# Kernel tuning notes

Hardware: AMD Instinct MI355X
Metric: run time of the kernel (lower is better)

The kernel has to match this reference:

```python
import jax, jax.numpy as jnp
import numpy as np

DIM = 512
HEADS = 8
TOP_K = 16


def setup_inputs() -> dict:
    key = jax.random.key(0)
    ks = jax.random.split(key, 7)
    B, N, C = 8, 1024, DIM
    std = 0.02
    return {
        "x": jax.random.normal(ks[0], (B, N, C), dtype=jnp.float32),
        "Wq": jax.random.normal(ks[1], (C, C), dtype=jnp.float32) * std,
        "bq": jnp.zeros((C,), dtype=jnp.float32),
        "Wkv": jax.random.normal(ks[2], (C, 2 * C), dtype=jnp.float32) * std,
        "bkv": jnp.zeros((2 * C,), dtype=jnp.float32),
        "Wp": jax.random.normal(ks[3], (C, C), dtype=jnp.float32) * std,
        "bp": jnp.zeros((C,), dtype=jnp.float32),
    }


def reference(x, Wq, bq, Wkv, bkv, Wp, bp):
    B, N, C = x.shape
    H = HEADS
    D = C // H
    scale = D ** (-0.5)

    # q: [B,H,N,D], ReLU-activated
    q = (x @ Wq + bq).reshape(B, N, H, D).transpose(0, 2, 1, 3)
    q = jax.nn.relu(q)
    # kv: [B,N,2,H,D] -> k,v each [B,H,N,D]
    kv = (x @ Wkv + bkv).reshape(B, N, 2, H, D).transpose(2, 0, 3, 1, 4)
    k, v = kv[0], kv[1]

    # dense scores [B,H,N,N]
    attn = jnp.einsum('bhnd,bhmd->bhnm', q, k) * scale

    # top-k mask along last dim (scatter ones at topk indices)
    _, idx = jax.lax.top_k(attn, TOP_K)            # [B,H,N,K]
    flat_attn = attn.reshape(-1, N)
    flat_idx = idx.reshape(-1, TOP_K)
    rows = jnp.arange(flat_attn.shape[0])[:, None]
    mask = jnp.zeros_like(flat_attn).at[rows, flat_idx].set(1.0).reshape(attn.shape)

    # NOTE: faithful to the original - softmax over the full row of attn*mask
    # (masked-out entries contribute exp(0)=1, exactly as in the torch code)
    sparse_attn = jax.nn.softmax(attn * mask, axis=-1)

    out = jnp.einsum('bhnm,bhmd->bhnd', sparse_attn, v)
    out = out.transpose(0, 2, 1, 3).reshape(B, N, C)
    out = out @ Wp + bp
    return out
```

## Files before the change

kernel.cpp:

```cpp
#include <hip/hip_runtime.h>
#include <float.h>

#define BATCH 8
#define SEQ   1024
#define CDIM  512
#define HEADS 8
#define HD    64
#define TOPK  16
#define MTOT  (BATCH*SEQ)

typedef short bf16x8 __attribute__((ext_vector_type(8)));
typedef float f32x4v __attribute__((ext_vector_type(4)));
typedef unsigned int __attribute__((address_space(1))) guint;
typedef unsigned int __attribute__((address_space(3))) luint;

__device__ inline void bf16split(float f, unsigned short& h, unsigned short& l) {
    unsigned u = __float_as_uint(f);
    unsigned hr = (u + 0x7fffu + ((u >> 16) & 1u)) >> 16;
    h = (unsigned short)hr;
    float rest = f - __uint_as_float(hr << 16);
    unsigned v = __float_as_uint(rest);
    l = (unsigned short)((v + 0x7fffu + ((v >> 16) & 1u)) >> 16);
}

__global__ __launch_bounds__(256) void split_x_kernel(
    const float* __restrict__ x,
    unsigned short* __restrict__ xhi, unsigned short* __restrict__ xlo)
{
    size_t i = ((size_t)blockIdx.x * 256 + threadIdx.x) * 4;
    float4 v = *(const float4*)(x + i);
    ushort4 h, l;
    bf16split(v.x, h.x, l.x); bf16split(v.y, h.y, l.y);
    bf16split(v.z, h.z, l.z); bf16split(v.w, h.w, l.w);
    *(ushort4*)(xhi + i) = h;
    *(ushort4*)(xlo + i) = l;
}

__global__ __launch_bounds__(256) void split_wT_kernel(
    const float* __restrict__ Wq, const float* __restrict__ Wkv,
    const float* __restrict__ Wp,
    unsigned short* __restrict__ bThi, unsigned short* __restrict__ bTlo,
    unsigned short* __restrict__ wpThi, unsigned short* __restrict__ wpTlo)
{
    __shared__ float tile[64][65];
    const int ct = blockIdx.x, k0 = blockIdx.y * 64, t = threadIdx.x;
    const float* src; int ld, sc0, dr0;
    unsigned short *dhi, *dlo;
    if (ct < 8)       { src = Wq;  ld = CDIM;     sc0 = ct * 64;        dr0 = ct * 64;              dhi = bThi;  dlo = bTlo;  }
    else if (ct < 24) { src = Wkv; ld = 2 * CDIM; sc0 = (ct - 8) * 64;  dr0 = CDIM + (ct - 8) * 64; dhi = bThi;  dlo = bTlo;  }
    else              { src = Wp;  ld = CDIM;     sc0 = (ct - 24) * 64; dr0 = (ct - 24) * 64;       dhi = wpThi; dlo = wpTlo; }

    #pragma unroll
    for (int i = 0; i < 4; i++) {
        int f = t + i * 256;
        int r = f >> 4, c4 = f & 15;
        float4 v = *(const float4*)(src + (size_t)(k0 + r) * ld + sc0 + c4 * 4);
        tile[c4*4+0][r] = v.x; tile[c4*4+1][r] = v.y;
        tile[c4*4+2][r] = v.z; tile[c4*4+3][r] = v.w;
    }
    __syncthreads();
    #pragma unroll
    for (int i = 0; i < 2; i++) {
        int f = t + i * 256;
        int c = f >> 3, ko = f & 7;
        const float* tp = &tile[c][ko * 8];
        ushort4 h0, l0, h1, l1;
        bf16split(tp[0], h0.x, l0.x); bf16split(tp[1], h0.y, l0.y);
        bf16split(tp[2], h0.z, l0.z); bf16split(tp[3], h0.w, l0.w);
        bf16split(tp[4], h1.x, l1.x); bf16split(tp[5], h1.y, l1.y);
        bf16split(tp[6], h1.z, l1.z); bf16split(tp[7], h1.w, l1.w);
        size_t o = (size_t)(dr0 + c) * CDIM + k0 + ko * 8;
        *(ushort4*)(dhi + o)     = h0; *(ushort4*)(dhi + o + 4) = h1;
        *(ushort4*)(dlo + o)     = l0; *(ushort4*)(dlo + o + 4) = l1;
    }
}

__device__ __forceinline__ void mfma_gemm_core(
    const unsigned short* __restrict__ ahi, const unsigned short* __restrict__ alo,
    const unsigned short* __restrict__ bhi, const unsigned short* __restrict__ blo,
    int row0, int col0, int lane, int w, f32x4v acc[4][4])
{
    __shared__ __align__(16) unsigned short ah_s[4096], al_s[4096];
    __shared__ __align__(16) unsigned short bh_s[4096], bl_s[4096];

    const unsigned short* gsrc;
    unsigned short* lbase;
    if (w == 0)      { gsrc = ahi; lbase = ah_s; }
    else if (w == 1) { gsrc = alo; lbase = al_s; }
    else if (w == 2) { gsrc = bhi; lbase = bh_s; }
    else             { gsrc = blo; lbase = bl_s; }
    const int tile0 = (w < 2) ? row0 : col0;
    const size_t goff = (size_t)(tile0 + (lane & 15)) * CDIM + (lane >> 4) * 8;
    const int wr = w >> 1, wc = w & 1;

    #pragma unroll
    for (int i = 0; i < 4; i++)
        #pragma unroll
        for (int j = 0; j < 4; j++)
            acc[i][j] = (f32x4v){0.f, 0.f, 0.f, 0.f};

    for (int kt = 0; kt < CDIM; kt += 32) {
        #pragma unroll
        for (int c = 0; c < 8; c++)
            __builtin_amdgcn_global_load_lds(
                (const guint*)(gsrc + goff + kt + (size_t)c * 16 * CDIM),
                (luint*)(lbase + c * 512), 16, 0, 0);
        __syncthreads();

        bf16x8 afh[4], afl[4], bfh[4], bfl[4];
        #pragma unroll
        for (int i = 0; i < 4; i++) {
            afh[i] = *(const bf16x8*)&ah_s[(((wr*4 + i) * 64) + lane) * 8];
            afl[i] = *(const bf16x8*)&al_s[(((wr*4 + i) * 64) + lane) * 8];
            bfh[i] = *(const bf16x8*)&bh_s[(((wc*4 + i) * 64) + lane) * 8];
            bfl[i] = *(const bf16x8*)&bl_s[(((wc*4 + i) * 64) + lane) * 8];
        }
        #pragma unroll
        for (int i = 0; i < 4; i++)
            #pragma unroll
            for (int j = 0; j < 4; j++) {
                acc[i][j] = __builtin_amdgcn_mfma_f32_16x16x32_bf16(bfh[j], afh[i], acc[i][j], 0, 0, 0);
                acc[i][j] = __builtin_amdgcn_mfma_f32_16x16x32_bf16(bfh[j], afl[i], acc[i][j], 0, 0, 0);
                acc[i][j] = __builtin_amdgcn_mfma_f32_16x16x32_bf16(bfl[j], afh[i], acc[i][j], 0, 0, 0);
            }
        __syncthreads();
    }
}

__global__ __launch_bounds__(256) void qkv_mfma_kernel(
    const unsigned short* __restrict__ xhi, const unsigned short* __restrict__ xlo,
    const unsigned short* __restrict__ bThi, const unsigned short* __restrict__ bTlo,
    const float* __restrict__ bq, const float* __restrict__ bkv,
    unsigned short* __restrict__ qhi_g, unsigned short* __restrict__ qlo_g,
    unsigned short* __restrict__ khi_g, unsigned short* __restrict__ klo_g,
    float* __restrict__ v_ws)
{
    const int tid = threadIdx.x, lane = tid & 63, w = tid >> 6;
    const int row0 = blockIdx.x * 128, col0 = blockIdx.y * 128;

    f32x4v acc[4][4];
    mfma_gemm_core(xhi, xlo, bThi, bTlo, row0, col0, lane, w, acc);

    const int wr = w >> 1, wc = w & 1;
    const bool isq = (col0 < CDIM);
    #pragma unroll
    for (int i = 0; i < 4; i++) {
        int rG = row0 + (wr*4 + i) * 16 + (lane & 15);
        int bb = rG >> 10, nn = rG & (SEQ - 1);
        #pragma unroll
        for (int j = 0; j < 4; j++) {
            int cG = col0 + (wc*4 + j) * 16 + (lane >> 4) * 4;
            float4 bias4 = isq ? *(const float4*)(bq + cG)
                               : *(const float4*)(bkv + cG - CDIM);
            float4 val;
            val.x = acc[i][j][0] + bias4.x;
            val.y = acc[i][j][1] + bias4.y;
            val.z = acc[i][j][2] + bias4.z;
            val.w = acc[i][j][3] + bias4.w;
            if (isq) {
                val.x = fmaxf(val.x, 0.f); val.y = fmaxf(val.y, 0.f);
                val.z = fmaxf(val.z, 0.f); val.w = fmaxf(val.w, 0.f);
                int hq = cG >> 6, d = cG & 63;
                size_t base = (((size_t)bb * HEADS + hq) * SEQ + nn) * HD + d;
                ushort4 hv, lv;
                bf16split(val.x, hv.x, lv.x); bf16split(val.y, hv.y, lv.y);
                bf16split(val.z, hv.z, lv.z); bf16split(val.w, hv.w, lv.w);
                *(ushort4*)(qhi_g + base) = hv;
                *(ushort4*)(qlo_g + base) = lv;
            } else {
                int c2 = cG - CDIM;
                int t = c2 >> 9, hq = (c2 >> 6) & 7, d = c2 & 63;
                size_t base = (((size_t)bb * HEADS + hq) * SEQ + nn) * HD + d;
                if (t == 0) {
                    ushort4 hv, lv;
                    bf16split(val.x, hv.x, lv.x); bf16split(val.y, hv.y, lv.y);
                    bf16split(val.z, hv.z, lv.z); bf16split(val.w, hv.w, lv.w);
                    *(ushort4*)(khi_g + base) = hv;
                    *(ushort4*)(klo_g + base) = lv;
                } else {
                    *(float4*)(v_ws + base) = val;
                }
            }
        }
    }
}

__global__ __launch_bounds__(256) void vsum_kernel(
    const float* __restrict__ v_ws, float* __restrict__ vsum_ws)
{
    __shared__ float red[4][HD];
    const int bh = blockIdx.x;
    const int d  = threadIdx.x & 63;
    const int sl = threadIdx.x >> 6;
    const float* vh = v_ws + (size_t)bh * SEQ * HD;
    float s = 0.f;
    for (int m = sl * 256; m < (sl + 1) * 256; m++) s += vh[(size_t)m * HD + d];
    red[sl][d] = s;
    __syncthreads();
    if (threadIdx.x < HD)
        vsum_ws[(size_t)bh * HD + d] = red[0][d] + red[1][d] + red[2][d] + red[3][d];
}

__global__ __launch_bounds__(256) void score_kernel(
    const unsigned short* __restrict__ qhi_g, const unsigned short* __restrict__ qlo_g,
    const unsigned short* __restrict__ khi_g, const unsigned short* __restrict__ klo_g,
    float* __restrict__ s_g, int bh0)
{
    __shared__ __align__(16) short qhi_s[4096], qlo_s[4096];
    __shared__ __align__(16) short khi_s[2][4096], klo_s[2][4096];

    const int bhl = blockIdx.y;
    const int bh  = bh0 + bhl;
    const int n0  = blockIdx.x * 64;
    const int tid = threadIdx.x;
    const int lane = tid & 63, w = tid >> 6;
    const int r_st = tid >> 2, c4 = tid & 3;
    const size_t hb = (size_t)bh * SEQ * HD;

    const int s0 = c4 * 2, s1 = s0 + 1;
    const int cx0 = ((r_st >> 4)*2 + (s0 >> 2))*64 + (s0 & 3)*16 + (r_st & 15);
    const int cx1 = ((r_st >> 4)*2 + (s1 >> 2))*64 + (s1 & 3)*16 + (r_st & 15);

    {
        const unsigned short* qp  = qhi_g + hb + (size_t)(n0 + r_st)*HD + c4*16;
        const unsigned short* qp2 = qlo_g + hb + (size_t)(n0 + r_st)*HD + c4*16;
        uint4 h0 = *(const uint4*)qp,  h1 = *(const uint4*)(qp + 8);
        uint4 l0 = *(const uint4*)qp2, l1 = *(const uint4*)(qp2 + 8);
        *(uint4*)&qhi_s[cx0*8] = h0; *(uint4*)&qhi_s[cx1*8] = h1;
        *(uint4*)&qlo_s[cx0*8] = l0; *(uint4*)&qlo_s[cx1*8] = l1;
    }
    __syncthreads();
    bf16x8 qh[2], ql[2];
    #pragma unroll
    for (int h = 0; h < 2; h++) {
        qh[h] = *(bf16x8*)&qhi_s[((w*2 + h)*64 + lane)*8];
        ql[h] = *(bf16x8*)&qlo_s[((w*2 + h)*64 + lane)*8];
    }

    {
        const unsigned short* kp  = khi_g + hb + (size_t)r_st*HD + c4*16;
        const unsigned short* kp2 = klo_g + hb + (size_t)r_st*HD + c4*16;
        uint4 kh0 = *(const uint4*)kp,  kh1 = *(const uint4*)(kp + 8);
        uint4 kl0 = *(const uint4*)kp2, kl1 = *(const uint4*)(kp2 + 8);
        *(uint4*)&khi_s[0][cx0*8] = kh0; *(uint4*)&khi_s[0][cx1*8] = kh1;
        *(uint4*)&klo_s[0][cx0*8] = kl0; *(uint4*)&klo_s[0][cx1*8] = kl1;
    }
    __syncthreads();

    float* srow_base = s_g + ((size_t)bhl << 20);

    for (int mt = 0; mt < SEQ / 64; mt++) {
        const int cur = mt & 1, nxt = cur ^ 1;
        uint4 kh0, kh1, kl0, kl1;
        if (mt + 1 < SEQ / 64) {
            const unsigned short* kp  = khi_g + hb + (size_t)((mt+1)*64 + r_st)*HD + c4*16;
            const unsigned short* kp2 = klo_g + hb + (size_t)((mt+1)*64 + r_st)*HD + c4*16;
            kh0 = *(const uint4*)kp;  kh1 = *(const uint4*)(kp + 8);
            kl0 = *(const uint4*)kp2; kl1 = *(const uint4*)(kp2 + 8);
        }

        #pragma unroll
        for (int ct = 0; ct < 4; ct++) {
            f32x4v acc = {0.f, 0.f, 0.f, 0.f};
            #pragma unroll
            for (int h = 0; h < 2; h++) {
                bf16x8 kfh = *(bf16x8*)&khi_s[cur][((ct*2 + h)*64 + lane)*8];
                bf16x8 kfl = *(bf16x8*)&klo_s[cur][((ct*2 + h)*64 + lane)*8];
                acc = __builtin_amdgcn_mfma_f32_16x16x32_bf16(qh[h], kfh, acc, 0, 0, 0);
                acc = __builtin_amdgcn_mfma_f32_16x16x32_bf16(qh[h], kfl, acc, 0, 0, 0);
                acc = __builtin_amdgcn_mfma_f32_16x16x32_bf16(ql[h], kfh, acc, 0, 0, 0);
            }
            const int col  = mt*64 + ct*16 + (lane & 15);
            const int rowb = n0 + w*16 + (lane >> 4)*4;
            float* sp = srow_base + ((size_t)rowb << 10) + col;
            #pragma unroll
            for (int rg = 0; rg < 4; rg++)
                sp[(size_t)rg << 10] = acc[rg] * 0.125f;
        }

        if (mt + 1 < SEQ / 64) {
            *(uint4*)&khi_s[nxt][cx0*8] = kh0; *(uint4*)&khi_s[nxt][cx1*8] = kh1;
            *(uint4*)&klo_s[nxt][cx0*8] = kl0; *(uint4*)&klo_s[nxt][cx1*8] = kl1;
        }
        __syncthreads();
    }
}

__device__ __forceinline__ unsigned long long packkey(float f, int gidx) {
    unsigned u = __float_as_uint(f);
    unsigned o = u ^ ((unsigned)((int)u >> 31) | 0x80000000u);
    return ((unsigned long long)o << 32) | (unsigned)(~gidx);
}

struct TopCache { unsigned long long t0, t1, t2, t3; int cnt; };

__device__ __forceinline__ void cache_insert(TopCache& c, unsigned long long k) {
    bool b0 = k > c.t0, b1 = k > c.t1, b2 = k > c.t2, b3 = k > c.t3;
    c.t3 = b3 ? (b2 ? c.t2 : k) : c.t3;
    c.t2 = b2 ? (b1 ? c.t1 : k) : c.t2;
    c.t1 = b1 ? (b0 ? c.t0 : k) : c.t1;
    c.t0 = b0 ? k : c.t0;
}

__device__ __forceinline__ void cache_build(TopCache& c, const float* v, int gbase) {
    c.t0 = c.t1 = c.t2 = c.t3 = 0ull;
    #pragma unroll
    for (int j = 0; j < 16; j++) cache_insert(c, packkey(v[j], gbase + j));
    c.cnt = 4;
}

__device__ __forceinline__ void cache_pop_own(TopCache& c, bool own) {
    c.t0 = own ? c.t1 : c.t0;
    c.t1 = own ? c.t2 : c.t1;
    c.t2 = own ? c.t3 : c.t2;
    c.t3 = own ? 0ull : c.t3;
    c.cnt -= own;
}

__device__ __forceinline__ void cache_refill(TopCache& c, const float* v,
                                             int gbase, unsigned long long kw) {
    c.t0 = c.t1 = c.t2 = c.t3 = 0ull;
    int cc = 0;
    #pragma unroll
    for (int j = 0; j < 16; j++) {
        unsigned long long k = packkey(v[j], gbase + j);
        if (k < kw) { cc++; cache_insert(c, k); }
    }
    c.cnt = cc > 4 ? 4 : cc;
}

__device__ __forceinline__ unsigned umax2(unsigned a, unsigned b) { return a > b ? a : b; }

__device__ __forceinline__ unsigned wave_max_ord(unsigned o) {
    unsigned p;
    p = (unsigned)__builtin_amdgcn_update_dpp(0, (int)o, 0xB1, 0xF, 0xF, true); o = umax2(o, p);
    p = (unsigned)__builtin_amdgcn_update_dpp(0, (int)o, 0x4E, 0xF, 0xF, true); o = umax2(o, p);
    p = (unsigned)__builtin_amdgcn_ds_swizzle((int)o, 0x101F); o = umax2(o, p);
    p = (unsigned)__builtin_amdgcn_ds_swizzle((int)o, 0x201F); o = umax2(o, p);
    p = (unsigned)__builtin_amdgcn_ds_swizzle((int)o, 0x401F); o = umax2(o, p);
    p = (unsigned)__shfl_xor((int)o, 32);                      o = umax2(o, p);
    return o;
}

__device__ __forceinline__ float ord_to_float(unsigned o) {
    return __uint_as_float(o ^ ((unsigned)((int)(~o) >> 31) | 0x80000000u));
}

__global__ __launch_bounds__(256) void topk_pv_kernel(
    const float* __restrict__ s_g, const float* __restrict__ v_ws,
    const float* __restrict__ vsum_ws,
    unsigned short* __restrict__ aohi, unsigned short* __restrict__ aolo, int bh0)
{
    const int lane = threadIdx.x & 63;
    const int wid  = (blockIdx.x * 256 + threadIdx.x) >> 6;
    const int bhl  = wid >> 9;
    const int pr   = wid & 511;
    const int nA   = pr * 2;
    const int bh   = bh0 + bhl;
    const int gbase = lane * 16;

    const float* srowA = s_g + ((size_t)bhl << 20) + ((size_t)nA << 10) + gbase;
    const float* srowB = srowA + SEQ;
    float vA[16], vB[16];
    #pragma unroll
    for (int i = 0; i < 4; i++) {
        float4 ta = *(const float4*)(srowA + i * 4);
        vA[i*4+0] = ta.x; vA[i*4+1] = ta.y; vA[i*4+2] = ta.z; vA[i*4+3] = ta.w;
        float4 tb = *(const float4*)(srowB + i * 4);
        vB[i*4+0] = tb.x; vB[i*4+1] = tb.y; vB[i*4+2] = tb.z; vB[i*4+3] = tb.w;
    }

    TopCache cA, cB;
    cache_build(cA, vA, gbase);
    cache_build(cB, vB, gbase);

    const float* vh = v_ws + ((size_t)bh << 16);
    const float vs = vsum_ws[(bh << 6) + lane];

    float mxA, eA, ZA, SA, mxB, eB, ZB, SB;

    {
        unsigned oA = (unsigned)(cA.t0 >> 32);
        unsigned oB = (unsigned)(cB.t0 >> 32);
        unsigned mA = wave_max_ord(oA);
        unsigned mB = wave_max_ord(oB);
        unsigned long long blA = __ballot(oA == mA);
        unsigned long long blB = __ballot(oB == mB);
        int sA = __ffsll(blA) - 1;
        int sB = __ffsll(blB) - 1;
        unsigned loA = (unsigned)__builtin_amdgcn_readlane((int)(unsigned)cA.t0, sA);
        unsigned loB = (unsigned)__builtin_amdgcn_readlane((int)(unsigned)cB.t0, sB);
        float valA = ord_to_float(mA), valB = ord_to_float(mB);
        int idxA = (int)((~loA) & 1023u);
        int idxB = (int)((~loB) & 1023u);

        mxA = fmaxf(valA, 0.f); eA = __expf(-mxA);
        float wEA = __expf(valA - mxA);
        ZA = (float)(SEQ - TOPK) * eA + wEA;
        SA = (wEA - eA) * vh[((size_t)idxA << 6) + lane];

        mxB = fmaxf(valB, 0.f); eB = __expf(-mxB);
        float wEB = __expf(valB - mxB);
        ZB = (float)(SEQ - TOPK) * eB + wEB;
        SB = (wEB - eB) * vh[((size_t)idxB << 6) + lane];

        cache_pop_own(cA, lane == sA);
        cache_pop_own(cB, lane == sB);
    }

    #pragma unroll 1
    for (int t = 1; t < TOPK; t++) {
        unsigned oA = (unsigned)(cA.t0 >> 32);
        unsigned oB = (unsigned)(cB.t0 >> 32);
        unsigned mA = wave_max_ord(oA);
        unsigned mB = wave_max_ord(oB);
        unsigned long long blA = __ballot(oA == mA);
        unsigned long long blB = __ballot(oB == mB);
        int sA = __ffsll(blA) - 1;
        int sB = __ffsll(blB) - 1;
        unsigned loA = (unsigned)__builtin_amdgcn_readlane((int)(unsigned)cA.t0, sA);
        unsigned loB = (unsigned)__builtin_amdgcn_readlane((int)(unsigned)cB.t0, sB);
        float valA = ord_to_float(mA), valB = ord_to_float(mB);
        int idxA = (int)((~loA) & 1023u);
        int idxB = (int)((~loB) & 1023u);

        float wEA = __expf(valA - mxA);
        ZA += wEA;
        SA = fmaf(wEA - eA, vh[((size_t)idxA << 6) + lane], SA);

        float wEB = __expf(valB - mxB);
        ZB += wEB;
        SB = fmaf(wEB - eB, vh[((size_t)idxB << 6) + lane], SB);

        cache_pop_own(cA, lane == sA);
        cache_pop_own(cB, lane == sB);

        if (cA.cnt == 0 && t < TOPK - 1) {
            unsigned long long kwA = ((unsigned long long)mA << 32) | loA;
            cache_refill(cA, vA, gbase, kwA);
        }
        if (cB.cnt == 0 && t < TOPK - 1) {
            unsigned long long kwB = ((unsigned long long)mB << 32) | loB;
            cache_refill(cB, vB, gbase, kwB);
        }
    }

    float accA = (eA * vs + SA) / ZA;
    float accB = (eB * vs + SB) / ZB;

    const int b = bh >> 3, hh = bh & 7;
    size_t oA = (((size_t)b << 10) + nA) * CDIM + (hh << 6) + lane;
    unsigned short sh, sl;
    bf16split(accA, sh, sl);
    aohi[oA] = sh; aolo[oA] = sl;
    bf16split(accB, sh, sl);
    aohi[oA + CDIM] = sh; aolo[oA + CDIM] = sl;
}

__global__ __launch_bounds__(256) void proj_mfma_kernel(
    const unsigned short* __restrict__ aohi, const unsigned short* __restrict__ aolo,
    const unsigned short* __restrict__ wpThi, const unsigned short* __restrict__ wpTlo,
    const float* __restrict__ bp, float* __restrict__ out)
{
    const int tid = threadIdx.x, lane = tid & 63, w = tid >> 6;
    const int row0 = blockIdx.x * 128, col0 = blockIdx.y * 128;

    f32x4v acc[4][4];
    mfma_gemm_core(aohi, aolo, wpThi, wpTlo, row0, col0, lane, w, acc);

    const int wr = w >> 1, wc = w & 1;
    #pragma unroll
    for (int i = 0; i < 4; i++) {
        int rG = row0 + (wr*4 + i) * 16 + (lane & 15);
        #pragma unroll
        for (int j = 0; j < 4; j++) {
            int cG = col0 + (wc*4 + j) * 16 + (lane >> 4) * 4;
            float4 b4 = *(const float4*)(bp + cG);
            float4 val;
            val.x = acc[i][j][0] + b4.x;
            val.y = acc[i][j][1] + b4.y;
            val.z = acc[i][j][2] + b4.z;
            val.w = acc[i][j][3] + b4.w;
            *(float4*)(out + (size_t)rG * CDIM + cG) = val;
        }
    }
}

extern "C" void kernel_launch(void* const* d_in, const int* in_sizes, int n_in,
                              void* d_out, int out_size, void* d_ws, size_t ws_size,
                              hipStream_t stream)
{
    const float* x   = (const float*)d_in[0];
    const float* Wq  = (const float*)d_in[1];
    const float* bq  = (const float*)d_in[2];
    const float* Wkv = (const float*)d_in[3];
    const float* bkv = (const float*)d_in[4];
    const float* Wp  = (const float*)d_in[5];
    const float* bp  = (const float*)d_in[6];
    float* out = (float*)d_out;

    const size_t HSZ = (size_t)BATCH * HEADS * SEQ * HD;
    float* ws    = (float*)d_ws;
    float* v_ws  = ws;
    float* vs_ws = ws + HSZ;
    unsigned short* qhi_g = (unsigned short*)(ws + HSZ + 4096);
    unsigned short* qlo_g = qhi_g + HSZ;
    unsigned short* khi_g = qhi_g + 2 * HSZ;
    unsigned short* klo_g = qhi_g + 3 * HSZ;
    unsigned short* xhi_g = qhi_g + 4 * HSZ;
    unsigned short* xlo_g = qhi_g + 5 * HSZ;
    unsigned short* bThi  = qhi_g + 6 * HSZ;
    unsigned short* bTlo  = bThi + (size_t)1536 * 512;
    unsigned short* wpThi = bThi + (size_t)2 * 1536 * 512;
    unsigned short* wpTlo = wpThi + (size_t)512 * 512;

    const size_t plane_us = 6 * HSZ + (size_t)2 * 1536 * 512 + (size_t)2 * 512 * 512;
    const size_t base_fl  = HSZ + 4096 + plane_us / 2;
    float* s_g = ws + base_fl;

    const size_t avail_fl = (ws_size / 4 > base_fl) ? (ws_size / 4 - base_fl) : 0;
    int G = 32;
    while (G > 1 && (size_t)G * SEQ * SEQ > avail_fl) G >>= 1;

    split_x_kernel<<<dim3((MTOT * CDIM) / (256 * 4)), 256, 0, stream>>>(x, xhi_g, xlo_g);
    split_wT_kernel<<<dim3(32, 8), 256, 0, stream>>>(Wq, Wkv, Wp, bThi, bTlo, wpThi, wpTlo);
    qkv_mfma_kernel<<<dim3(MTOT / 128, 12), 256, 0, stream>>>(
        xhi_g, xlo_g, bThi, bTlo, bq, bkv, qhi_g, qlo_g, khi_g, klo_g, v_ws);
    vsum_kernel<<<BATCH * HEADS, 256, 0, stream>>>(v_ws, vs_ws);
    for (int bh0 = 0; bh0 < BATCH * HEADS; bh0 += G) {
        score_kernel<<<dim3(SEQ / 64, G), 256, 0, stream>>>(
            qhi_g, qlo_g, khi_g, klo_g, s_g, bh0);
        topk_pv_kernel<<<dim3(G * (SEQ / 8)), 256, 0, stream>>>(
            s_g, v_ws, vs_ws, xhi_g, xlo_g, bh0);
    }
    proj_mfma_kernel<<<dim3(MTOT / 128, CDIM / 128), 256, 0, stream>>>(
        xhi_g, xlo_g, wpThi, wpTlo, bp, out);
}
```

Baseline: 362.0 us.

## Double-buffer LDS tiles in MFMA GEMM core to overlap loads with compute

Doubles the shared-memory A/B hi/lo tile buffers and prefetches the next K-slice with global_load_lds while the MFMAs consume the current slice. This replaces the two __syncthreads per iteration with a single explicit vmcnt wait and barrier, hiding global-load latency behind compute. It doubles LDS use of the GEMM core to 64 KB, which may lower occupancy.

```diff
diff --git a/kernel.cpp b/kernel.cpp
--- a/kernel.cpp
+++ b/kernel.cpp
@@ -80,15 +80,15 @@
     const unsigned short* __restrict__ bhi, const unsigned short* __restrict__ blo,
     int row0, int col0, int lane, int w, f32x4v acc[4][4])
 {
-    __shared__ __align__(16) unsigned short ah_s[4096], al_s[4096];
-    __shared__ __align__(16) unsigned short bh_s[4096], bl_s[4096];
+    __shared__ __align__(16) unsigned short ah_s[2][4096], al_s[2][4096];
+    __shared__ __align__(16) unsigned short bh_s[2][4096], bl_s[2][4096];
 
     const unsigned short* gsrc;
-    unsigned short* lbase;
-    if (w == 0)      { gsrc = ahi; lbase = ah_s; }
-    else if (w == 1) { gsrc = alo; lbase = al_s; }
-    else if (w == 2) { gsrc = bhi; lbase = bh_s; }
-    else             { gsrc = blo; lbase = bl_s; }
+    unsigned short* lb[2];
+    if (w == 0)      { gsrc = ahi; lb[0] = ah_s[0]; lb[1] = ah_s[1]; }
+    else if (w == 1) { gsrc = alo; lb[0] = al_s[0]; lb[1] = al_s[1]; }
+    else if (w == 2) { gsrc = bhi; lb[0] = bh_s[0]; lb[1] = bh_s[1]; }
+    else             { gsrc = blo; lb[0] = bl_s[0]; lb[1] = bl_s[1]; }
     const int tile0 = (w < 2) ? row0 : col0;
     const size_t goff = (size_t)(tile0 + (lane & 15)) * CDIM + (lane >> 4) * 8;
     const int wr = w >> 1, wc = w & 1;
@@ -99,21 +99,36 @@
         for (int j = 0; j < 4; j++)
             acc[i][j] = (f32x4v){0.f, 0.f, 0.f, 0.f};
 
+    #pragma unroll
+    for (int c = 0; c < 8; c++)
+        __builtin_amdgcn_global_load_lds(
+            (const guint*)(gsrc + goff + (size_t)c * 16 * CDIM),
+            (luint*)(lb[0] + c * 512), 16, 0, 0);
+    asm volatile("s_waitcnt vmcnt(0)" ::: "memory");
+    __builtin_amdgcn_s_barrier();
+
+    int cur = 0;
     for (int kt = 0; kt < CDIM; kt += 32) {
-        #pragma unroll
-        for (int c = 0; c < 8; c++)
-            __builtin_amdgcn_global_load_lds(
-                (const guint*)(gsrc + goff + kt + (size_t)c * 16 * CDIM),
-                (luint*)(lbase + c * 512), 16, 0, 0);
-        __syncthreads();
-
+        if (kt + 32 < CDIM) {
+            unsigned short* ln = lb[cur ^ 1];
+            #pragma unroll
+            for (int c = 0; c < 8; c++)
+                __builtin_amdgcn_global_load_lds(
+                    (const guint*)(gsrc + goff + kt + 32 + (size_t)c * 16 * CDIM),
+                    (luint*)(ln + c * 512), 16, 0, 0);
+        }
+
+        const unsigned short* ah = ah_s[cur];
+        const unsigned short* al = al_s[cur];
+        const unsigned short* bh = bh_s[cur];
+        const unsigned short* bl = bl_s[cur];
         bf16x8 afh[4], afl[4], bfh[4], bfl[4];
         #pragma unroll
         for (int i = 0; i < 4; i++) {
-            afh[i] = *(const bf16x8*)&ah_s[(((wr*4 + i) * 64) + lane) * 8];
-            afl[i] = *(const bf16x8*)&al_s[(((wr*4 + i) * 64) + lane) * 8];
-            bfh[i] = *(const bf16x8*)&bh_s[(((wc*4 + i) * 64) + lane) * 8];
-            bfl[i] = *(const bf16x8*)&bl_s[(((wc*4 + i) * 64) + lane) * 8];
+            afh[i] = *(const bf16x8*)&ah[(((wr*4 + i) * 64) + lane) * 8];
+            afl[i] = *(const bf16x8*)&al[(((wr*4 + i) * 64) + lane) * 8];
+            bfh[i] = *(const bf16x8*)&bh[(((wc*4 + i) * 64) + lane) * 8];
+            bfl[i] = *(const bf16x8*)&bl[(((wc*4 + i) * 64) + lane) * 8];
         }
         #pragma unroll
         for (int i = 0; i < 4; i++)
@@ -123,7 +138,11 @@
                 acc[i][j] = __builtin_amdgcn_mfma_f32_16x16x32_bf16(bfh[j], afl[i], acc[i][j], 0, 0, 0);
                 acc[i][j] = __builtin_amdgcn_mfma_f32_16x16x32_bf16(bfl[j], afh[i], acc[i][j], 0, 0, 0);
             }
-        __syncthreads();
+
+        __builtin_amdgcn_sched_barrier(0);
+        asm volatile("s_waitcnt vmcnt(0)" ::: "memory");
+        __builtin_amdgcn_s_barrier();
+        cur ^= 1;
     }
 }
 
```

Measured after the change: 346.5 us. -4.3%, faster.

## Load GEMM fragments directly from global into registers with double buffering

Applied to the files above, without the earlier changes.

Replaces the shared-memory staging in the split-bf16 MFMA GEMM core, where each wave copied one operand tile with global_load_lds and synchronized, with per-wave direct global loads of fragments into registers. Two register buffers are ping-ponged so the next K-slice loads while the current one feeds the MFMAs, and the __syncthreads are removed. The launch bounds also request 2 blocks per SM. The cost is redundant global and L2 traffic, since waves sharing a row or column tile now each load it, and higher register pressure from the double-buffered fragments.

```diff
diff --git a/kernel.cpp b/kernel.cpp
--- a/kernel.cpp
+++ b/kernel.cpp
@@ -11,8 +11,6 @@
 
 typedef short bf16x8 __attribute__((ext_vector_type(8)));
 typedef float f32x4v __attribute__((ext_vector_type(4)));
-typedef unsigned int __attribute__((address_space(1))) guint;
-typedef unsigned int __attribute__((address_space(3))) luint;
 
 __device__ inline void bf16split(float f, unsigned short& h, unsigned short& l) {
     unsigned u = __float_as_uint(f);
@@ -75,23 +73,43 @@
     }
 }
 
+__device__ __forceinline__ void ld_frag4(uint4* d, const unsigned short* p) {
+    d[0] = *(const uint4*)(p);
+    d[1] = *(const uint4*)(p + 16 * CDIM);
+    d[2] = *(const uint4*)(p + 32 * CDIM);
+    d[3] = *(const uint4*)(p + 48 * CDIM);
+}
+
+__device__ __forceinline__ void mfma_step(
+    const uint4* ah, const uint4* al, const uint4* bh, const uint4* bl,
+    f32x4v acc[4][4])
+{
+    #pragma unroll
+    for (int i = 0; i < 4; i++) {
+        bf16x8 afh = *(const bf16x8*)&ah[i];
+        bf16x8 afl = *(const bf16x8*)&al[i];
+        #pragma unroll
+        for (int j = 0; j < 4; j++) {
+            bf16x8 bfh = *(const bf16x8*)&bh[j];
+            bf16x8 bfl = *(const bf16x8*)&bl[j];
+            acc[i][j] = __builtin_amdgcn_mfma_f32_16x16x32_bf16(bfh, afh, acc[i][j], 0, 0, 0);
+            acc[i][j] = __builtin_amdgcn_mfma_f32_16x16x32_bf16(bfh, afl, acc[i][j], 0, 0, 0);
+            acc[i][j] = __builtin_amdgcn_mfma_f32_16x16x32_bf16(bfl, afh, acc[i][j], 0, 0, 0);
+        }
+    }
+}
+
 __device__ __forceinline__ void mfma_gemm_core(
     const unsigned short* __restrict__ ahi, const unsigned short* __restrict__ alo,
     const unsigned short* __restrict__ bhi, const unsigned short* __restrict__ blo,
     int row0, int col0, int lane, int w, f32x4v acc[4][4])
 {
-    __shared__ __align__(16) unsigned short ah_s[4096], al_s[4096];
-    __shared__ __align__(16) unsigned short bh_s[4096], bl_s[4096];
-
-    const unsigned short* gsrc;
-    unsigned short* lbase;
-    if (w == 0)      { gsrc = ahi; lbase = ah_s; }
-    else if (w == 1) { gsrc = alo; lbase = al_s; }
-    else if (w == 2) { gsrc = bhi; lbase = bh_s; }
-    else             { gsrc = blo; lbase = bl_s; }
-    const int tile0 = (w < 2) ? row0 : col0;
-    const size_t goff = (size_t)(tile0 + (lane & 15)) * CDIM + (lane >> 4) * 8;
     const int wr = w >> 1, wc = w & 1;
+    const int lrow = lane & 15, koct = (lane >> 4) * 8;
+    const unsigned short* pah = ahi + (size_t)(row0 + wr * 64 + lrow) * CDIM + koct;
+    const unsigned short* pal = alo + (size_t)(row0 + wr * 64 + lrow) * CDIM + koct;
+    const unsigned short* pbh = bhi + (size_t)(col0 + wc * 64 + lrow) * CDIM + koct;
+    const unsigned short* pbl = blo + (size_t)(col0 + wc * 64 + lrow) * CDIM + koct;
 
     #pragma unroll
     for (int i = 0; i < 4; i++)
@@ -99,35 +117,25 @@
         for (int j = 0; j < 4; j++)
             acc[i][j] = (f32x4v){0.f, 0.f, 0.f, 0.f};
 
-    for (int kt = 0; kt < CDIM; kt += 32) {
-        #pragma unroll
-        for (int c = 0; c < 8; c++)
-            __builtin_amdgcn_global_load_lds(
-                (const guint*)(gsrc + goff + kt + (size_t)c * 16 * CDIM),
-                (luint*)(lbase + c * 512), 16, 0, 0);
-        __syncthreads();
-
-        bf16x8 afh[4], afl[4], bfh[4], bfl[4];
-        #pragma unroll
-        for (int i = 0; i < 4; i++) {
-            afh[i] = *(const bf16x8*)&ah_s[(((wr*4 + i) * 64) + lane) * 8];
-            afl[i] = *(const bf16x8*)&al_s[(((wr*4 + i) * 64) + lane) * 8];
-            bfh[i] = *(const bf16x8*)&bh_s[(((wc*4 + i) * 64) + lane) * 8];
-            bfl[i] = *(const bf16x8*)&bl_s[(((wc*4 + i) * 64) + lane) * 8];
-        }
-        #pragma unroll
-        for (int i = 0; i < 4; i++)
-            #pragma unroll
-            for (int j = 0; j < 4; j++) {
-                acc[i][j] = __builtin_amdgcn_mfma_f32_16x16x32_bf16(bfh[j], afh[i], acc[i][j], 0, 0, 0);
-                acc[i][j] = __builtin_amdgcn_mfma_f32_16x16x32_bf16(bfh[j], afl[i], acc[i][j], 0, 0, 0);
-                acc[i][j] = __builtin_amdgcn_mfma_f32_16x16x32_bf16(bfl[j], afh[i], acc[i][j], 0, 0, 0);
-            }
-        __syncthreads();
-    }
-}
-
-__global__ __launch_bounds__(256) void qkv_mfma_kernel(
+    uint4 cah[4], cal_[4], cbh[4], cbl_[4];
+    uint4 nah[4], nal_[4], nbh[4], nbl_[4];
+
+    ld_frag4(cah, pah);  ld_frag4(cal_, pal);
+    ld_frag4(cbh, pbh);  ld_frag4(cbl_, pbl);
+
+    for (int kt = 0; kt < CDIM; kt += 64) {
+        ld_frag4(nah, pah + kt + 32);  ld_frag4(nal_, pal + kt + 32);
+        ld_frag4(nbh, pbh + kt + 32);  ld_frag4(nbl_, pbl + kt + 32);
+        mfma_step(cah, cal_, cbh, cbl_, acc);
+        if (kt + 64 < CDIM) {
+            ld_frag4(cah, pah + kt + 64);  ld_frag4(cal_, pal + kt + 64);
+            ld_frag4(cbh, pbh + kt + 64);  ld_frag4(cbl_, pbl + kt + 64);
+        }
+        mfma_step(nah, nal_, nbh, nbl_, acc);
+    }
+}
+
+__global__ __launch_bounds__(256, 2) void qkv_mfma_kernel(
     const unsigned short* __restrict__ xhi, const unsigned short* __restrict__ xlo,
     const unsigned short* __restrict__ bThi, const unsigned short* __restrict__ bTlo,
     const float* __restrict__ bq, const float* __restrict__ bkv,
@@ -457,7 +465,7 @@
     aohi[oA + CDIM] = sh; aolo[oA + CDIM] = sl;
 }
 
-__global__ __launch_bounds__(256) void proj_mfma_kernel(
+__global__ __launch_bounds__(256, 2) void proj_mfma_kernel(
     const unsigned short* __restrict__ aohi, const unsigned short* __restrict__ aolo,
     const unsigned short* __restrict__ wpThi, const unsigned short* __restrict__ wpTlo,
     const float* __restrict__ bp, float* __restrict__ out)
```

After: 392.7 us. +8.5%, slower.
